# Kernel tuning notes

Hardware: AMD Instinct MI355X
Metric: run time of the kernel (lower is better)

## Reference

```python
import jax, jax.numpy as jnp
import numpy as np

B, LQ, LK, D, H, DK, DV = 4, 2048, 2048, 1024, 16, 64, 64
TEMP = float(np.sqrt(DK))
LN_EPS = 1e-5


def setup_inputs() -> dict:
    key = jax.random.key(0)
    ks = jax.random.split(key, 12)
    std_qk = float(np.sqrt(2.0 / (D + DK)))
    std_v = float(np.sqrt(2.0 / (D + DV)))
    std_fc = float(np.sqrt(2.0 / (H * DV + D)))  # xavier normal
    return {
        "q": jax.random.normal(ks[0], (B, LQ, D), jnp.float32),
        "k": jax.random.normal(ks[1], (B, LK, D), jnp.float32),
        "v": jax.random.normal(ks[2], (B, LK, D), jnp.float32),
        "key_padding_mask": jax.random.randint(ks[3], (B, LK), 0, 2) > 0,
        "Wq": jax.random.normal(ks[4], (D, H * DK), jnp.float32) * std_qk,
        "bq": jnp.zeros((H * DK,), jnp.float32),
        "Wk": jax.random.normal(ks[5], (D, H * DK), jnp.float32) * std_qk,
        "bk": jnp.zeros((H * DK,), jnp.float32),
        "Wv": jax.random.normal(ks[6], (D, H * DV), jnp.float32) * std_v,
        "bv": jnp.zeros((H * DV,), jnp.float32),
        "Wo": jax.random.normal(ks[7], (H * DV, D), jnp.float32) * std_fc,
        "bo": jnp.zeros((D,), jnp.float32),
        "ln_g": jnp.ones((D,), jnp.float32),
        "ln_b": jnp.zeros((D,), jnp.float32),
    }


def reference(q, k, v, key_padding_mask, Wq, bq, Wk, bk, Wv, bv, Wo, bo, ln_g, ln_b):
    residual = q
    # projections -> [B, H, L, dh]
    qh = (q @ Wq + bq).reshape(B, LQ, H, DK).transpose(0, 2, 1, 3)
    kh = (k @ Wk + bk).reshape(B, LK, H, DK).transpose(0, 2, 1, 3)
    vh = (v @ Wv + bv).reshape(B, LK, H, DV).transpose(0, 2, 1, 3)
    # scaled dot-product attention, mask padded keys with -inf pre-softmax
    logits = jnp.einsum("bhqd,bhkd->bhqk", qh, kh) / TEMP
    logits = jnp.where(key_padding_mask[:, None, None, :], -jnp.inf, logits)
    attn = jax.nn.softmax(logits, axis=-1)  # masked entries -> 0
    out = jnp.einsum("bhqk,bhkd->bhqd", attn, vh)
    # concat heads (head-major per original permute) -> [B, LQ, H*DV]
    out = out.transpose(0, 2, 1, 3).reshape(B, LQ, H * DV)
    out = out @ Wo + bo
    out = out + residual  # skip connection (d_out == d_model)
    # LayerNorm over last dim
    mu = out.mean(-1, keepdims=True)
    var = ((out - mu) ** 2).mean(-1, keepdims=True)
    out = (out - mu) * jax.lax.rsqrt(var + LN_EPS) * ln_g + ln_b
    attn_avg = attn.mean(axis=1)  # average over heads -> [B, LQ, LK]
    return out, attn_avg
```

## Files before the change

### kernel.cpp

```cpp
#include <hip/hip_runtime.h>
#include <hip/hip_bf16.h>
#include <math.h>

#define B_    4
#define LQ_   2048
#define LK_   2048
#define D_    1024
#define H_    16
#define LN_EPS_ 1e-5f
#define NEGINF (-__builtin_inff())
#define QSCALE 0.18033688011112042f

typedef __attribute__((ext_vector_type(8))) short bf16x8;
typedef __attribute__((ext_vector_type(4))) short bf16x4;
typedef __attribute__((ext_vector_type(4))) float f32x4;

#define MFMA(a, b, c) __builtin_amdgcn_mfma_f32_16x16x32_bf16(a, b, c, 0, 0, 0)

#if __has_builtin(__builtin_amdgcn_exp2f)
#define EXP2(x) __builtin_amdgcn_exp2f(x)
#else
#define EXP2(x) __expf((x) * 0.6931471805599453f)
#endif

__device__ __forceinline__ short f2bf(float f) {
    union { __hip_bfloat16 h; short s; } u;
    u.h = __float2bfloat16(f);
    return u.s;
}

__device__ __forceinline__ void gld16(const short* g, short* l) {
    __builtin_amdgcn_global_load_lds(
        (const __attribute__((address_space(1))) void*)g,
        (__attribute__((address_space(3))) void*)l, 16, 0, 0);
}

__device__ __forceinline__ void xcd_swz(int gx, int n8, int* bx, int* by) {
    const int lin = *bx + gx * (*by);
    const int nl  = (lin & 7) * n8 + (lin >> 3);
    *bx = nl % gx;
    *by = nl / gx;
}

__global__ __launch_bounds__(256) void scan_kernel(
    const int* __restrict__ mask, int* __restrict__ idx, int* __restrict__ pos,
    int* __restrict__ cnt, float* __restrict__ maskc)
{
    const int b = blockIdx.x;
    const int t = threadIdx.x;
    const int lane = t & 63, wid = t >> 6;
    __shared__ int wsum[4];
    const int base = b * 2048 + t * 8;

    int fl[8]; int loc = 0;
    #pragma unroll
    for (int j = 0; j < 8; ++j) { fl[j] = (mask[base + j] == 0) ? 1 : 0; loc += fl[j]; }

    int inc = loc;
    #pragma unroll
    for (int d = 1; d < 64; d <<= 1) {
        const int n = __shfl_up(inc, d);
        if (lane >= d) inc += n;
    }
    if (lane == 63) wsum[wid] = inc;
    __syncthreads();
    int wbase = 0;
    for (int i = 0; i < wid; ++i) wbase += wsum[i];
    const int total = wsum[0] + wsum[1] + wsum[2] + wsum[3];

    int e = wbase + inc - loc;
    #pragma unroll
    for (int j = 0; j < 8; ++j) {
        const int p = t * 8 + j;
        if (fl[j]) { idx[b * 2048 + e] = p; pos[base + j] = e; ++e; }
        else        pos[base + j] = -1;
        maskc[base + j] = (p < total) ? 0.f : NEGINF;
        if (p >= total) idx[base + j] = 0;
    }
    if (t == 0) cnt[b] = total;
}

__global__ __launch_bounds__(256) void cast_x_kernel(
    const float* __restrict__ q, const float* __restrict__ k, const float* __restrict__ v,
    const int* __restrict__ mask,
    short* __restrict__ Xq, short* __restrict__ Xk, short* __restrict__ Xv,
    float* __restrict__ maskf)
{
    const int which = blockIdx.y;
    const float* src = which == 0 ? q : (which == 1 ? k : v);
    short* dst       = which == 0 ? Xq : (which == 1 ? Xk : Xv);
    const int t = threadIdx.x;
    const size_t i = ((size_t)blockIdx.x * 256 + t) * 8;
    const float4 a = *reinterpret_cast<const float4*>(src + i);
    const float4 c = *reinterpret_cast<const float4*>(src + i + 4);
    bf16x8 o;
    o[0] = f2bf(a.x); o[1] = f2bf(a.y); o[2] = f2bf(a.z); o[3] = f2bf(a.w);
    o[4] = f2bf(c.x); o[5] = f2bf(c.y); o[6] = f2bf(c.z); o[7] = f2bf(c.w);
    *reinterpret_cast<bf16x8*>(dst + i) = o;
    if (which == 0) {
        const int gid = blockIdx.x * 256 + t;
        if (gid < B_ * LK_) maskf[gid] = (mask[gid] != 0) ? NEGINF : 0.0f;
    }
}

__global__ __launch_bounds__(256) void cast_wt_kernel(
    const float* __restrict__ Wq, const float* __restrict__ Wk,
    const float* __restrict__ Wv, const float* __restrict__ Wo,
    short* __restrict__ Wtq, short* __restrict__ Wtk,
    short* __restrict__ Wtv, short* __restrict__ Wto)
{
    const int which = blockIdx.z;
    const float* W = which == 0 ? Wq : (which == 1 ? Wk : (which == 2 ? Wv : Wo));
    short* Wt      = which == 0 ? Wtq : (which == 1 ? Wtk : (which == 2 ? Wtv : Wto));

    __shared__ float T[64][65];
    const int t = threadIdx.x;
    const int k0 = blockIdx.x * 64, n0 = blockIdx.y * 64;
    {
        const int row = t >> 2, cq = (t & 3) * 16;
        #pragma unroll
        for (int i = 0; i < 4; ++i) {
            const float4 v4 = *reinterpret_cast<const float4*>(&W[(size_t)(k0 + row) * 1024 + n0 + cq + i * 4]);
            T[row][cq + i * 4 + 0] = v4.x; T[row][cq + i * 4 + 1] = v4.y;
            T[row][cq + i * 4 + 2] = v4.z; T[row][cq + i * 4 + 3] = v4.w;
        }
    }
    __syncthreads();
    const int nl = t >> 2, kq = (t & 3) * 16;
    bf16x8 o0, o1;
    #pragma unroll
    for (int j = 0; j < 8; ++j) {
        o0[j] = f2bf(T[kq + j][nl]);
        o1[j] = f2bf(T[kq + 8 + j][nl]);
    }
    *reinterpret_cast<bf16x8*>(&Wt[(size_t)(n0 + nl) * 1024 + k0 + kq]) = o0;
    *reinterpret_cast<bf16x8*>(&Wt[(size_t)(n0 + nl) * 1024 + k0 + kq + 8]) = o1;
}

__global__ __launch_bounds__(256) void proj_kernel(
    const short* __restrict__ Xq, const short* __restrict__ Xk, const short* __restrict__ Xv,
    const short* __restrict__ Wtq, const short* __restrict__ Wtk, const short* __restrict__ Wtv,
    const float* __restrict__ bq, const float* __restrict__ bk, const float* __restrict__ bv,
    const int* __restrict__ pos,
    short* __restrict__ qh, short* __restrict__ kh, short* __restrict__ vTc)
{
    const int which = blockIdx.z;
    const short* A  = which == 0 ? Xq : (which == 1 ? Xk : Xv);
    const short* Bt = which == 0 ? Wtq : (which == 1 ? Wtk : Wtv);
    const float* bias = which == 0 ? bq : (which == 1 ? bk : bv);

    __shared__ short Al[4096];
    __shared__ short Bl[4096];

    const int t = threadIdx.x;
    const int lane = t & 63, w = t >> 6;
    const int wm = w >> 1, wn = w & 1;
    const int g = lane >> 4, r16 = lane & 15;

    int bx = blockIdx.x, by = blockIdx.y;
    xcd_swz(8, 64, &bx, &by);
    const int m0 = by * 128, n0 = bx * 128;

    f32x4 acc[4][4] = {};

    for (int k0 = 0; k0 < 1024; k0 += 32) {
        __syncthreads();
        #pragma unroll
        for (int i = 0; i < 2; ++i) {
            const int row = i * 64 + (t >> 2);
            const int cl = (t & 3) ^ ((row >> 1) & 3);
            gld16(A  + (size_t)(m0 + row) * 1024 + k0 + cl * 8, Al + i * 2048 + t * 8);
            gld16(Bt + (size_t)(n0 + row) * 1024 + k0 + cl * 8, Bl + i * 2048 + t * 8);
        }
        __syncthreads();

        bf16x8 af[4], bf[4];
        #pragma unroll
        for (int mf = 0; mf < 4; ++mf) {
            const int row = wm * 64 + mf * 16 + r16;
            af[mf] = *reinterpret_cast<const bf16x8*>(
                (const char*)Al + row * 64 + (((g ^ ((row >> 1) & 3))) << 4));
        }
        #pragma unroll
        for (int nf = 0; nf < 4; ++nf) {
            const int row = wn * 64 + nf * 16 + r16;
            bf[nf] = *reinterpret_cast<const bf16x8*>(
                (const char*)Bl + row * 64 + (((g ^ ((row >> 1) & 3))) << 4));
        }
        #pragma unroll
        for (int mf = 0; mf < 4; ++mf)
            #pragma unroll
            for (int nf = 0; nf < 4; ++nf)
                acc[mf][nf] = MFMA(af[mf], bf[nf], acc[mf][nf]);
    }

    if (which < 2) {
        #pragma unroll
        for (int nf = 0; nf < 4; ++nf) {
            const int n = n0 + wn * 64 + nf * 16 + r16;
            const int h = n >> 6, dh = n & 63;
            const float bn = bias[n];
            #pragma unroll
            for (int mf = 0; mf < 4; ++mf) {
                #pragma unroll
                for (int r = 0; r < 4; ++r) {
                    const int m = m0 + wm * 64 + mf * 16 + 4 * g + r;
                    const int bb = m >> 11, l = m & 2047;
                    float vf = acc[mf][nf][r] + bn;
                    if (which == 0) vf *= QSCALE;
                    ((which == 0) ? qh : kh)[(((size_t)(bb * H_ + h)) * LQ_ + l) * 64 + dh] = f2bf(vf);
                }
            }
        }
    } else {
        int posr[4][4], bbr[4][4];
        #pragma unroll
        for (int mf = 0; mf < 4; ++mf)
            #pragma unroll
            for (int r = 0; r < 4; ++r) {
                const int m = m0 + wm * 64 + mf * 16 + 4 * g + r;
                const int bb = m >> 11, l = m & 2047;
                bbr[mf][r] = bb;
                posr[mf][r] = pos[bb * 2048 + l];
            }
        #pragma unroll
        for (int nf = 0; nf < 4; ++nf) {
            const int n = n0 + wn * 64 + nf * 16 + r16;
            const int h = n >> 6, dh = n & 63;
            const float bn = bias[n];
            #pragma unroll
            for (int mf = 0; mf < 4; ++mf) {
                #pragma unroll
                for (int r = 0; r < 4; ++r) {
                    const int pc = posr[mf][r];
                    if (pc >= 0)
                        vTc[(((size_t)(bbr[mf][r] * H_ + h)) * 64 + dh) * (size_t)LK_ + pc] =
                            f2bf(acc[mf][nf][r] + bn);
                }
            }
        }
    }
}

__global__ __launch_bounds__(512) void flash_kernel(
    const short* __restrict__ qh, const short* __restrict__ kh, const short* __restrict__ vTc,
    const int* __restrict__ idx, const int* __restrict__ cnt, const float* __restrict__ maskc,
    short* __restrict__ ctx, float* __restrict__ mOut, float* __restrict__ sOut)
{
    int bx = blockIdx.x, by = blockIdx.y;
    xcd_swz(16, 32, &bx, &by);
    const int q0 = bx * 128;
    const int h  = by;
    const int b  = blockIdx.z;

    __shared__ short Kl[2][4096];
    __shared__ short Vl[2][4096];

    const int t = threadIdx.x;
    const int lane = t & 63, w = t >> 6;
    const int g = lane >> 4, q16 = lane & 15;

    const short* kbase = kh + (size_t)(b * H_ + h) * LK_ * 64;
    const short* vbase = vTc + (size_t)(b * H_ + h) * 64 * (size_t)LK_;
    const int*   idxb  = idx + b * 2048;
    const int nt = (cnt[b] + 63) >> 6;

    bf16x8 qf0, qf1;
    {
        const short* qrow = qh + ((size_t)(b * H_ + h) * LQ_ + q0 + w * 16 + q16) * 64;
        qf0 = *reinterpret_cast<const bf16x8*>(qrow + 8 * g);
        qf1 = *reinterpret_cast<const bf16x8*>(qrow + 32 + 8 * g);
    }

    f32x4 mlast[4] = {};
    if (nt > 0) {
        #pragma unroll
        for (int kb = 0; kb < 4; ++kb)
            mlast[kb] = *reinterpret_cast<const f32x4*>(
                maskc + b * 2048 + (nt - 1) * 64 + kb * 16 + 4 * g);
    }

    const int srw = t >> 3, scl = t & 7;
    const int cl = scl ^ (srw & 7);

    f32x4 ot[4] = {};
    float m_run = NEGINF, l_run = 0.f;

    if (nt > 0) {
        const int orig = idxb[srw];
        gld16(kbase + (size_t)orig * 64 + cl * 8, Kl[0] + t * 8);
        gld16(vbase + (size_t)srw * LK_ + cl * 8, Vl[0] + t * 8);
    }
    __syncthreads();

    int cur = 0;
    for (int kt = 0; kt < nt; ++kt) {
        if (kt + 1 < nt) {
            const int kn = (kt + 1) * 64;
            const int orig = idxb[kn + srw];
            gld16(kbase + (size_t)orig * 64 + cl * 8, Kl[cur ^ 1] + t * 8);
            gld16(vbase + (size_t)srw * LK_ + kn + cl * 8, Vl[cur ^ 1] + t * 8);
        }
        const bool lastt = (kt == nt - 1);

        float lg[4][4];
        const short* klp = Kl[cur];
        __builtin_amdgcn_s_setprio(1);
        #pragma unroll
        for (int kb = 0; kb < 4; ++kb) {
            const int krow = kb * 16 + q16;
            const char* rowp = (const char*)klp + krow * 128;
            const int sw = (krow & 7) << 4;
            const bf16x8 kf0 = *reinterpret_cast<const bf16x8*>(rowp + ((g << 4) ^ sw));
            const bf16x8 kf1 = *reinterpret_cast<const bf16x8*>(rowp + (((4 + g) << 4) ^ sw));
            f32x4 s = lastt ? mlast[kb] : (f32x4){0.f, 0.f, 0.f, 0.f};
            s = MFMA(kf0, qf0, s);
            s = MFMA(kf1, qf1, s);
            #pragma unroll
            for (int r = 0; r < 4; ++r) lg[kb][r] = s[r];
        }
        __builtin_amdgcn_s_setprio(0);

        float tm = NEGINF;
        #pragma unroll
        for (int kb = 0; kb < 4; ++kb)
            #pragma unroll
            for (int r = 0; r < 4; ++r) tm = fmaxf(tm, lg[kb][r]);
        tm = fmaxf(tm, __shfl_xor(tm, 16));
        tm = fmaxf(tm, __shfl_xor(tm, 32));

        const bool skip = __all(tm <= m_run + 8.0f);
        if (!skip) {
            const float m_new = fmaxf(m_run, tm);
            const float alpha = (m_run == NEGINF) ? 0.f : EXP2(m_run - m_new);
            #pragma unroll
            for (int fc = 0; fc < 4; ++fc)
                #pragma unroll
                for (int r = 0; r < 4; ++r) ot[fc][r] *= alpha;
            l_run *= alpha;
            m_run = m_new;
        }
        const float m_use = (m_run == NEGINF) ? 0.f : m_run;

        float p[4][4];
        float ls = 0.f;
        #pragma unroll
        for (int kb = 0; kb < 4; ++kb)
            #pragma unroll
            for (int r = 0; r < 4; ++r) { p[kb][r] = EXP2(lg[kb][r] - m_use); ls += p[kb][r]; }
        ls += __shfl_xor(ls, 16);
        ls += __shfl_xor(ls, 32);
        l_run += ls;

        bf16x8 pb[2];
        #pragma unroll
        for (int r = 0; r < 4; ++r) {
            pb[0][r]     = f2bf(p[0][r]);
            pb[0][4 + r] = f2bf(p[1][r]);
            pb[1][r]     = f2bf(p[2][r]);
            pb[1][4 + r] = f2bf(p[3][r]);
        }

        const short* vlp = Vl[cur];
        __builtin_amdgcn_s_setprio(1);
        #pragma unroll
        for (int fc = 0; fc < 4; ++fc) {
            const int dvrow = fc * 16 + q16;
            const char* rowp = (const char*)vlp + dvrow * 128;
            const int sw = (dvrow & 7) << 4;
            #pragma unroll
            for (int tt = 0; tt < 2; ++tt) {
                const bf16x4 va = *reinterpret_cast<const bf16x4*>(rowp + ((64 * tt + 8 * g) ^ sw));
                const bf16x4 vb = *reinterpret_cast<const bf16x4*>(rowp + ((64 * tt + 32 + 8 * g) ^ sw));
                bf16x8 af;
                af[0] = va[0]; af[1] = va[1]; af[2] = va[2]; af[3] = va[3];
                af[4] = vb[0]; af[5] = vb[1]; af[6] = vb[2]; af[7] = vb[3];
                ot[fc] = MFMA(af, pb[tt], ot[fc]);
            }
        }
        __builtin_amdgcn_s_setprio(0);

        __syncthreads();
        cur ^= 1;
    }

    const float rs = (l_run > 0.f) ? 1.0f / l_run : 0.f;
    short* crow = ctx + ((size_t)b * LQ_ + q0 + w * 16 + q16) * (size_t)(H_ * 64) + h * 64;
    #pragma unroll
    for (int fc = 0; fc < 4; ++fc) {
        bf16x4 o4;
        #pragma unroll
        for (int r = 0; r < 4; ++r) o4[r] = f2bf(ot[fc][r] * rs);
        *reinterpret_cast<bf16x4*>(crow + fc * 16 + 4 * g) = o4;
    }
    if (lane < 16) {
        const size_t idxo = (size_t)(b * H_ + h) * LQ_ + q0 + w * 16 + lane;
        mOut[idxo] = m_run;
        sOut[idxo] = l_run;
    }
}

__global__ __launch_bounds__(512) void avg_kernel(
    const short* __restrict__ qh, const short* __restrict__ kh,
    const float* __restrict__ maskf,
    const float* __restrict__ mS, const float* __restrict__ sS,
    float* __restrict__ attn_avg)
{
    const int k0 = blockIdx.x * 64;
    const int q0 = blockIdx.y * 128;
    const int b  = blockIdx.z;

    __shared__ short Kl[2][4096];

    const int t = threadIdx.x;
    const int lane = t & 63, w = t >> 6;
    const int g = lane >> 4, q16 = lane & 15;

    f32x4 mk[4];
    #pragma unroll
    for (int kb = 0; kb < 4; ++kb)
        mk[kb] = *reinterpret_cast<const f32x4*>(maskf + b * LK_ + k0 + kb * 16 + 4 * g);

    const int srw = t >> 3, scl = t & 7;
    const int cl = scl ^ (srw & 7);
    const short* kbb = kh + ((size_t)b * H_ * LK_ + k0) * 64;

    const short* qbase = qh + ((size_t)b * H_ * LQ_ + q0 + w * 16 + q16) * 64;
    const size_t stbase = (size_t)b * H_ * LQ_ + q0 + w * 16 + q16;

    {
        gld16(kbb + (size_t)srw * 64 + cl * 8, Kl[0] + t * 8);
    }
    bf16x8 qc0 = *reinterpret_cast<const bf16x8*>(qbase + 8 * g);
    bf16x8 qc1 = *reinterpret_cast<const bf16x8*>(qbase + 32 + 8 * g);
    float mc = mS[stbase], sc = sS[stbase];
    __syncthreads();

    f32x4 acc[4] = {};
    int cur = 0;
    for (int hh = 0; hh < H_; ++hh) {
        bf16x8 qn0, qn1; float mn = 0.f, sn = 0.f;
        if (hh + 1 < H_) {
            gld16(kbb + (size_t)(hh + 1) * LK_ * 64 + (size_t)srw * 64 + cl * 8,
                  Kl[cur ^ 1] + t * 8);
            const short* qp = qbase + (size_t)(hh + 1) * LQ_ * 64;
            qn0 = *reinterpret_cast<const bf16x8*>(qp + 8 * g);
            qn1 = *reinterpret_cast<const bf16x8*>(qp + 32 + 8 * g);
            mn = mS[stbase + (size_t)(hh + 1) * LQ_];
            sn = sS[stbase + (size_t)(hh + 1) * LQ_];
        }

        const float madj = (mc == NEGINF || sc <= 0.f)
                               ? __builtin_inff() : mc + __log2f(sc);

        const short* klp = Kl[cur];
        __builtin_amdgcn_s_setprio(1);
        #pragma unroll
        for (int kb = 0; kb < 4; ++kb) {
            const int krow = kb * 16 + q16;
            const char* rowp = (const char*)klp + krow * 128;
            const int sw = (krow & 7) << 4;
            const bf16x8 kf0 = *reinterpret_cast<const bf16x8*>(rowp + ((g << 4) ^ sw));
            const bf16x8 kf1 = *reinterpret_cast<const bf16x8*>(rowp + (((4 + g) << 4) ^ sw));
            f32x4 s = mk[kb];
            s = MFMA(kf0, qc0, s);
            s = MFMA(kf1, qc1, s);
            #pragma unroll
            for (int r = 0; r < 4; ++r)
                acc[kb][r] += EXP2(s[r] - madj);
        }
        __builtin_amdgcn_s_setprio(0);

        __syncthreads();
        if (hh + 1 < H_) { qc0 = qn0; qc1 = qn1; mc = mn; sc = sn; }
        cur ^= 1;
    }

    const float scale = 1.0f / (float)H_;
    float* orow = attn_avg + ((size_t)b * LQ_ + q0 + w * 16 + q16) * (size_t)LK_ + k0;
    #pragma unroll
    for (int kb = 0; kb < 4; ++kb) {
        f32x4 o = acc[kb];
        o[0] *= scale; o[1] *= scale; o[2] *= scale; o[3] *= scale;
        *reinterpret_cast<f32x4*>(orow + kb * 16 + 4 * g) = o;
    }
}

__global__ __launch_bounds__(256) void outproj_kernel(
    const short* __restrict__ ctxIn, const short* __restrict__ Wto,
    const float* __restrict__ bo, const float* __restrict__ resid,
    float* __restrict__ preln)
{
    __shared__ short Al[4096];
    __shared__ short Bl[4096];

    const int t = threadIdx.x;
    const int lane = t & 63, w = t >> 6;
    const int wm = w >> 1, wn = w & 1;
    const int g = lane >> 4, r16 = lane & 15;

    int bx = blockIdx.x, by = blockIdx.y;
    xcd_swz(8, 64, &bx, &by);
    const int m0 = by * 128, n0 = bx * 128;

    f32x4 acc[4][4] = {};

    for (int k0 = 0; k0 < 1024; k0 += 32) {
        __syncthreads();
        #pragma unroll
        for (int i = 0; i < 2; ++i) {
            const int row = i * 64 + (t >> 2);
            const int cl = (t & 3) ^ ((row >> 1) & 3);
            gld16(ctxIn + (size_t)(m0 + row) * 1024 + k0 + cl * 8, Al + i * 2048 + t * 8);
            gld16(Wto   + (size_t)(n0 + row) * 1024 + k0 + cl * 8, Bl + i * 2048 + t * 8);
        }
        __syncthreads();

        bf16x8 af[4], bf[4];
        #pragma unroll
        for (int mf = 0; mf < 4; ++mf) {
            const int row = wm * 64 + mf * 16 + r16;
            af[mf] = *reinterpret_cast<const bf16x8*>(
                (const char*)Al + row * 64 + (((g ^ ((row >> 1) & 3))) << 4));
        }
        #pragma unroll
        for (int nf = 0; nf < 4; ++nf) {
            const int row = wn * 64 + nf * 16 + r16;
            bf[nf] = *reinterpret_cast<const bf16x8*>(
                (const char*)Bl + row * 64 + (((g ^ ((row >> 1) & 3))) << 4));
        }
        #pragma unroll
        for (int mf = 0; mf < 4; ++mf)
            #pragma unroll
            for (int nf = 0; nf < 4; ++nf)
                acc[mf][nf] = MFMA(af[mf], bf[nf], acc[mf][nf]);
    }

    #pragma unroll
    for (int nf = 0; nf < 4; ++nf) {
        const int n = n0 + wn * 64 + nf * 16 + r16;
        const float bn = bo[n];
        #pragma unroll
        for (int mf = 0; mf < 4; ++mf) {
            #pragma unroll
            for (int r = 0; r < 4; ++r) {
                const size_t m = m0 + wm * 64 + mf * 16 + 4 * g + r;
                preln[m * 1024 + n] = acc[mf][nf][r] + bn + resid[m * 1024 + n];
            }
        }
    }
}

__global__ __launch_bounds__(256) void ln_kernel(
    const float* __restrict__ xin, const float* __restrict__ gam,
    const float* __restrict__ bet, float* __restrict__ out)
{
    const size_t row = blockIdx.x;
    const int t = threadIdx.x;
    const float4 v = *reinterpret_cast<const float4*>(&xin[row * 1024 + t * 4]);

    float s  = v.x + v.y + v.z + v.w;
    float ss = v.x * v.x + v.y * v.y + v.z * v.z + v.w * v.w;
    #pragma unroll
    for (int w = 1; w < 64; w <<= 1) { s += __shfl_xor(s, w); ss += __shfl_xor(ss, w); }

    __shared__ float rs_[4], rss_[4];
    if ((t & 63) == 0) { rs_[t >> 6] = s; rss_[t >> 6] = ss; }
    __syncthreads();
    s  = rs_[0] + rs_[1] + rs_[2] + rs_[3];
    ss = rss_[0] + rss_[1] + rss_[2] + rss_[3];

    const float mean = s * (1.0f / 1024.0f);
    const float var  = ss * (1.0f / 1024.0f) - mean * mean;
    const float rstd = rsqrtf(var + LN_EPS_);

    const float4 g4 = *reinterpret_cast<const float4*>(&gam[t * 4]);
    const float4 b4 = *reinterpret_cast<const float4*>(&bet[t * 4]);
    float4 o;
    o.x = (v.x - mean) * rstd * g4.x + b4.x;
    o.y = (v.y - mean) * rstd * g4.y + b4.y;
    o.z = (v.z - mean) * rstd * g4.z + b4.z;
    o.w = (v.w - mean) * rstd * g4.w + b4.w;
    *reinterpret_cast<float4*>(&out[row * 1024 + t * 4]) = o;
}

extern "C" void kernel_launch(void* const* d_in, const int* in_sizes, int n_in,
                              void* d_out, int out_size, void* d_ws, size_t ws_size,
                              hipStream_t stream)
{
    const float* q    = (const float*)d_in[0];
    const float* k    = (const float*)d_in[1];
    const float* v    = (const float*)d_in[2];
    const int*   mask = (const int*)d_in[3];
    const float* Wq   = (const float*)d_in[4];
    const float* bq   = (const float*)d_in[5];
    const float* Wk   = (const float*)d_in[6];
    const float* bk   = (const float*)d_in[7];
    const float* Wv   = (const float*)d_in[8];
    const float* bv   = (const float*)d_in[9];
    const float* Wo   = (const float*)d_in[10];
    const float* bo   = (const float*)d_in[11];
    const float* lng  = (const float*)d_in[12];
    const float* lnb  = (const float*)d_in[13];

    float* out      = (float*)d_out;
    float* attn_avg = out + (size_t)B_ * LQ_ * D_;

    const size_t XSZ = (size_t)B_ * LQ_ * D_;
    const size_t WSZ = (size_t)D_ * D_;

    short* Xq  = (short*)d_ws;
    short* Xk  = Xq + XSZ;
    short* Xv  = Xk + XSZ;
    short* Wtq = Xv + XSZ;
    short* Wtk = Wtq + WSZ;
    short* Wtv = Wtk + WSZ;
    short* Wto = Wtv + WSZ;
    short* qh  = Wto + WSZ;
    short* kh  = qh + XSZ;
    short* vTc = kh + XSZ;
    float* mSt = (float*)(vTc + XSZ);
    float* sSt = mSt + (size_t)B_ * H_ * LQ_;
    float* maskf = sSt + (size_t)B_ * H_ * LQ_;
    float* maskc = maskf + (size_t)B_ * LK_;
    int*   idx   = (int*)(maskc + (size_t)B_ * LK_);
    int*   pos   = idx + (size_t)B_ * LK_;
    int*   cnt   = pos + (size_t)B_ * LK_;
    float* preln = (float*)qh;
    short* ctx   = Xv;

    scan_kernel<<<dim3(B_), 256, 0, stream>>>(mask, idx, pos, cnt, maskc);
    cast_x_kernel<<<dim3(4096, 3), 256, 0, stream>>>(q, k, v, mask, Xq, Xk, Xv, maskf);
    cast_wt_kernel<<<dim3(16, 16, 4), 256, 0, stream>>>(Wq, Wk, Wv, Wo, Wtq, Wtk, Wtv, Wto);

    proj_kernel<<<dim3(8, 64, 3), 256, 0, stream>>>(Xq, Xk, Xv, Wtq, Wtk, Wtv,
                                                    bq, bk, bv, pos, qh, kh, vTc);

    flash_kernel<<<dim3(16, 16, 4), 512, 0, stream>>>(qh, kh, vTc, idx, cnt, maskc,
                                                      ctx, mSt, sSt);

    avg_kernel<<<dim3(32, 16, 4), 512, 0, stream>>>(qh, kh, maskf, mSt, sSt, attn_avg);

    outproj_kernel<<<dim3(8, 64), 256, 0, stream>>>(ctx, Wto, bo, q, preln);

    ln_kernel<<<8192, 256, 0, stream>>>(preln, lng, lnb, out);
}
```

Baseline: 307.1 us.

## Fuse fp32-to-bf16 input cast into projection GEMM and store pre-LN as bf16

Removes the separate activation cast kernel. The projection GEMM now loads fp32 q/k/v tiles straight into LDS through a swizzled layout and converts them to bf16 in registers before the MFMA. The mask-float computation moves into the scan kernel. The pre-LayerNorm buffer is now stored as bf16 instead of fp32, halving that round trip. In exchange, each GEMM reads twice the bytes per A tile from global memory, uses more LDS, and does conversions in the inner loop. The bf16 pre-LN storage lowers output precision.

```diff
diff --git a/kernel.cpp b/kernel.cpp
--- a/kernel.cpp
+++ b/kernel.cpp
@@ -29,6 +29,12 @@
     return u.s;
 }
 
+__device__ __forceinline__ float bf2f(short s) {
+    union { float f; unsigned u; } z;
+    z.u = ((unsigned)(unsigned short)s) << 16;
+    return z.f;
+}
+
 __device__ __forceinline__ void gld16(const short* g, short* l) {
     __builtin_amdgcn_global_load_lds(
         (const __attribute__((address_space(1))) void*)g,
@@ -44,7 +50,7 @@
 
 __global__ __launch_bounds__(256) void scan_kernel(
     const int* __restrict__ mask, int* __restrict__ idx, int* __restrict__ pos,
-    int* __restrict__ cnt, float* __restrict__ maskc)
+    int* __restrict__ cnt, float* __restrict__ maskc, float* __restrict__ maskf)
 {
     const int b = blockIdx.x;
     const int t = threadIdx.x;
@@ -75,32 +81,10 @@
         if (fl[j]) { idx[b * 2048 + e] = p; pos[base + j] = e; ++e; }
         else        pos[base + j] = -1;
         maskc[base + j] = (p < total) ? 0.f : NEGINF;
+        maskf[base + j] = fl[j] ? 0.f : NEGINF;
         if (p >= total) idx[base + j] = 0;
     }
     if (t == 0) cnt[b] = total;
-}
-
-__global__ __launch_bounds__(256) void cast_x_kernel(
-    const float* __restrict__ q, const float* __restrict__ k, const float* __restrict__ v,
-    const int* __restrict__ mask,
-    short* __restrict__ Xq, short* __restrict__ Xk, short* __restrict__ Xv,
-    float* __restrict__ maskf)
-{
-    const int which = blockIdx.y;
-    const float* src = which == 0 ? q : (which == 1 ? k : v);
-    short* dst       = which == 0 ? Xq : (which == 1 ? Xk : Xv);
-    const int t = threadIdx.x;
-    const size_t i = ((size_t)blockIdx.x * 256 + t) * 8;
-    const float4 a = *reinterpret_cast<const float4*>(src + i);
-    const float4 c = *reinterpret_cast<const float4*>(src + i + 4);
-    bf16x8 o;
-    o[0] = f2bf(a.x); o[1] = f2bf(a.y); o[2] = f2bf(a.z); o[3] = f2bf(a.w);
-    o[4] = f2bf(c.x); o[5] = f2bf(c.y); o[6] = f2bf(c.z); o[7] = f2bf(c.w);
-    *reinterpret_cast<bf16x8*>(dst + i) = o;
-    if (which == 0) {
-        const int gid = blockIdx.x * 256 + t;
-        if (gid < B_ * LK_) maskf[gid] = (mask[gid] != 0) ? NEGINF : 0.0f;
-    }
 }
 
 __global__ __launch_bounds__(256) void cast_wt_kernel(
@@ -138,18 +122,18 @@
 }
 
 __global__ __launch_bounds__(256) void proj_kernel(
-    const short* __restrict__ Xq, const short* __restrict__ Xk, const short* __restrict__ Xv,
+    const float* __restrict__ Xq, const float* __restrict__ Xk, const float* __restrict__ Xv,
     const short* __restrict__ Wtq, const short* __restrict__ Wtk, const short* __restrict__ Wtv,
     const float* __restrict__ bq, const float* __restrict__ bk, const float* __restrict__ bv,
     const int* __restrict__ pos,
     short* __restrict__ qh, short* __restrict__ kh, short* __restrict__ vTc)
 {
     const int which = blockIdx.z;
-    const short* A  = which == 0 ? Xq : (which == 1 ? Xk : Xv);
+    const float* A  = which == 0 ? Xq : (which == 1 ? Xk : Xv);
     const short* Bt = which == 0 ? Wtq : (which == 1 ? Wtk : Wtv);
     const float* bias = which == 0 ? bq : (which == 1 ? bk : bv);
 
-    __shared__ short Al[4096];
+    __shared__ float AlF[4096];
     __shared__ short Bl[4096];
 
     const int t = threadIdx.x;
@@ -166,10 +150,17 @@
     for (int k0 = 0; k0 < 1024; k0 += 32) {
         __syncthreads();
         #pragma unroll
+        for (int j = 0; j < 4; ++j) {
+            const int c = j * 256 + t;
+            const int row = c >> 3, col = c & 7;
+            const int scol = col ^ (row & 7);
+            gld16((const short*)(A + (size_t)(m0 + row) * 1024 + k0 + scol * 4),
+                  (short*)AlF + (size_t)c * 8);
+        }
+        #pragma unroll
         for (int i = 0; i < 2; ++i) {
             const int row = i * 64 + (t >> 2);
             const int cl = (t & 3) ^ ((row >> 1) & 3);
-            gld16(A  + (size_t)(m0 + row) * 1024 + k0 + cl * 8, Al + i * 2048 + t * 8);
             gld16(Bt + (size_t)(n0 + row) * 1024 + k0 + cl * 8, Bl + i * 2048 + t * 8);
         }
         __syncthreads();
@@ -178,8 +169,14 @@
         #pragma unroll
         for (int mf = 0; mf < 4; ++mf) {
             const int row = wm * 64 + mf * 16 + r16;
-            af[mf] = *reinterpret_cast<const bf16x8*>(
-                (const char*)Al + row * 64 + (((g ^ ((row >> 1) & 3))) << 4));
+            const int c0 = (2 * g) ^ (row & 7);
+            const int c1 = (2 * g + 1) ^ (row & 7);
+            const f32x4 a0 = *reinterpret_cast<const f32x4*>(AlF + row * 32 + c0 * 4);
+            const f32x4 a1 = *reinterpret_cast<const f32x4*>(AlF + row * 32 + c1 * 4);
+            bf16x8 a8;
+            #pragma unroll
+            for (int r = 0; r < 4; ++r) { a8[r] = f2bf(a0[r]); a8[4 + r] = f2bf(a1[r]); }
+            af[mf] = a8;
         }
         #pragma unroll
         for (int nf = 0; nf < 4; ++nf) {
@@ -489,7 +486,7 @@
 __global__ __launch_bounds__(256) void outproj_kernel(
     const short* __restrict__ ctxIn, const short* __restrict__ Wto,
     const float* __restrict__ bo, const float* __restrict__ resid,
-    float* __restrict__ preln)
+    short* __restrict__ preln)
 {
     __shared__ short Al[4096];
     __shared__ short Bl[4096];
@@ -545,22 +542,25 @@
             #pragma unroll
             for (int r = 0; r < 4; ++r) {
                 const size_t m = m0 + wm * 64 + mf * 16 + 4 * g + r;
-                preln[m * 1024 + n] = acc[mf][nf][r] + bn + resid[m * 1024 + n];
+                preln[m * 1024 + n] = f2bf(acc[mf][nf][r] + bn + resid[m * 1024 + n]);
             }
         }
     }
 }
 
 __global__ __launch_bounds__(256) void ln_kernel(
-    const float* __restrict__ xin, const float* __restrict__ gam,
+    const short* __restrict__ xin, const float* __restrict__ gam,
     const float* __restrict__ bet, float* __restrict__ out)
 {
     const size_t row = blockIdx.x;
     const int t = threadIdx.x;
-    const float4 v = *reinterpret_cast<const float4*>(&xin[row * 1024 + t * 4]);
-
-    float s  = v.x + v.y + v.z + v.w;
-    float ss = v.x * v.x + v.y * v.y + v.z * v.z + v.w * v.w;
+    const bf16x4 pv = *reinterpret_cast<const bf16x4*>(&xin[row * 1024 + t * 4]);
+    float x[4];
+    #pragma unroll
+    for (int j = 0; j < 4; ++j) x[j] = bf2f(pv[j]);
+
+    float s  = x[0] + x[1] + x[2] + x[3];
+    float ss = x[0] * x[0] + x[1] * x[1] + x[2] * x[2] + x[3] * x[3];
     #pragma unroll
     for (int w = 1; w < 64; w <<= 1) { s += __shfl_xor(s, w); ss += __shfl_xor(ss, w); }
 
@@ -577,10 +577,10 @@
     const float4 g4 = *reinterpret_cast<const float4*>(&gam[t * 4]);
     const float4 b4 = *reinterpret_cast<const float4*>(&bet[t * 4]);
     float4 o;
-    o.x = (v.x - mean) * rstd * g4.x + b4.x;
-    o.y = (v.y - mean) * rstd * g4.y + b4.y;
-    o.z = (v.z - mean) * rstd * g4.z + b4.z;
-    o.w = (v.w - mean) * rstd * g4.w + b4.w;
+    o.x = (x[0] - mean) * rstd * g4.x + b4.x;
+    o.y = (x[1] - mean) * rstd * g4.y + b4.y;
+    o.z = (x[2] - mean) * rstd * g4.z + b4.z;
+    o.w = (x[3] - mean) * rstd * g4.w + b4.w;
     *reinterpret_cast<float4*>(&out[row * 1024 + t * 4]) = o;
 }
 
@@ -609,10 +609,8 @@
     const size_t XSZ = (size_t)B_ * LQ_ * D_;
     const size_t WSZ = (size_t)D_ * D_;
 
-    short* Xq  = (short*)d_ws;
-    short* Xk  = Xq + XSZ;
-    short* Xv  = Xk + XSZ;
-    short* Wtq = Xv + XSZ;
+    short* Xpad = (short*)d_ws;
+    short* Wtq = Xpad + 3 * XSZ;
     short* Wtk = Wtq + WSZ;
     short* Wtv = Wtk + WSZ;
     short* Wto = Wtv + WSZ;
@@ -626,14 +624,13 @@
     int*   idx   = (int*)(maskc + (size_t)B_ * LK_);
     int*   pos   = idx + (size_t)B_ * LK_;
     int*   cnt   = pos + (size_t)B_ * LK_;
-    float* preln = (float*)qh;
-    short* ctx   = Xv;
-
-    scan_kernel<<<dim3(B_), 256, 0, stream>>>(mask, idx, pos, cnt, maskc);
-    cast_x_kernel<<<dim3(4096, 3), 256, 0, stream>>>(q, k, v, mask, Xq, Xk, Xv, maskf);
+    short* preln = qh;
+    short* ctx   = Xpad;
+
+    scan_kernel<<<dim3(B_), 256, 0, stream>>>(mask, idx, pos, cnt, maskc, maskf);
     cast_wt_kernel<<<dim3(16, 16, 4), 256, 0, stream>>>(Wq, Wk, Wv, Wo, Wtq, Wtk, Wtv, Wto);
 
-    proj_kernel<<<dim3(8, 64, 3), 256, 0, stream>>>(Xq, Xk, Xv, Wtq, Wtk, Wtv,
+    proj_kernel<<<dim3(8, 64, 3), 256, 0, stream>>>(q, k, v, Wtq, Wtk, Wtv,
                                                     bq, bk, bv, pos, qh, kh, vTc);
 
     flash_kernel<<<dim3(16, 16, 4), 512, 0, stream>>>(qh, kh, vTc, idx, cnt, maskc,
```

Measured after the change: 316.1 us. 1.03x slower.
